# Kernel tuning notes

Measured on AMD Instinct MI355X. Metric: run time of the kernel, lower is better.

Reference implementation:

```python
import jax, jax.numpy as jnp
import numpy as np
import math

D_MODEL = 1024
NUM_HEADS = 16
HEAD_DIM = D_MODEL // NUM_HEADS


def _xavier(key, out_f, in_f):
    limit = math.sqrt(6.0 / (in_f + out_f))
    return jax.random.uniform(key, (out_f, in_f), jnp.float32, -limit, limit)


def ternarize(w):
    # abs-mean threshold -> {-1, 0, +1}
    abs_mean = jnp.mean(jnp.abs(w))
    return jnp.where(jnp.abs(w) > abs_mean, jnp.sign(w), jnp.zeros_like(w))


def setup_inputs() -> dict:
    key = jax.random.key(0)
    kq, kk, kv, kwq, kwk, kwv, kwo = jax.random.split(key, 7)
    B, S = 2, 2048
    return {
        "query": jax.random.normal(kq, (B, S, D_MODEL), jnp.float32),
        "key": jax.random.normal(kk, (B, S, D_MODEL), jnp.float32),
        "value": jax.random.normal(kv, (B, S, D_MODEL), jnp.float32),
        "w_q": _xavier(kwq, D_MODEL, D_MODEL),
        "w_k": _xavier(kwk, D_MODEL, D_MODEL),
        "w_v": _xavier(kwv, D_MODEL, D_MODEL),
        "w_o": _xavier(kwo, D_MODEL, D_MODEL),
    }


def reference(query, key, value, w_q, w_k, w_v, w_o):
    B, S, _ = query.shape
    # ternary projections (F.linear: x @ W.T)
    q = query @ ternarize(w_q).T
    k = key @ ternarize(w_k).T
    v = value @ ternarize(w_v).T
    # [B, H, S, Dh]
    q = q.reshape(B, S, NUM_HEADS, HEAD_DIM).transpose(0, 2, 1, 3)
    k = k.reshape(B, -1, NUM_HEADS, HEAD_DIM).transpose(0, 2, 1, 3)
    v = v.reshape(B, -1, NUM_HEADS, HEAD_DIM).transpose(0, 2, 1, 3)
    scores = jnp.einsum("bhqd,bhkd->bhqk", q, k) / math.sqrt(HEAD_DIM)
    probs = jax.nn.softmax(scores, axis=-1)
    out = jnp.einsum("bhqk,bhkd->bhqd", probs, v)
    out = out.transpose(0, 2, 1, 3).reshape(B, S, D_MODEL)
    return out @ ternarize(w_o).T
```

## Files before the change

kernel.cpp:

```cpp
#include <hip/hip_runtime.h>
#include <cstdint>
#include <cstddef>

typedef __bf16 bfloat;
typedef __bf16 bf16x8 __attribute__((ext_vector_type(8)));
typedef __bf16 bf16x4 __attribute__((ext_vector_type(4)));
typedef float  f32x4  __attribute__((ext_vector_type(4)));

static constexpr int D  = 1024;
static constexpr int S  = 2048;
static constexpr int B  = 2;
static constexpr int H  = 16;
static constexpr int DH = 64;
static constexpr int M  = B * S;
static constexpr int WMAT_N = 1024 * 1024;

#define MFMA_BF16(a, b, c) __builtin_amdgcn_mfma_f32_16x16x32_bf16((a), (b), (c), 0, 0, 0)

__device__ __forceinline__ void gl_lds16(const void* g, void* l) {
  __builtin_amdgcn_global_load_lds(
      (const __attribute__((address_space(1))) void*)g,
      (__attribute__((address_space(3))) void*)l, 16, 0, 0);
}

__global__ void prep_kernel(const float* __restrict__ w0, const float* __restrict__ w1,
                            const float* __restrict__ w2, const float* __restrict__ w3,
                            const float* __restrict__ qx, const float* __restrict__ kx,
                            const float* __restrict__ vx, bfloat* __restrict__ qhi,
                            bfloat* __restrict__ qlo, bfloat* __restrict__ khi,
                            bfloat* __restrict__ klo, bfloat* __restrict__ vhi,
                            double* __restrict__ sums) {
  const int y = blockIdx.y;
  if (y < 4) {
    const float* w = (y == 0) ? w0 : (y == 1) ? w1 : (y == 2) ? w2 : w3;
    const float4* w4 = (const float4*)w;
    double s = 0.0;
    for (int i = blockIdx.x * blockDim.x + threadIdx.x; i < (WMAT_N / 4);
         i += gridDim.x * blockDim.x) {
      float4 v = w4[i];
      s += (double)fabsf(v.x) + (double)fabsf(v.y) + (double)fabsf(v.z) + (double)fabsf(v.w);
    }
    for (int off = 1; off < 64; off <<= 1) s += __shfl_xor(s, off, 64);
    __shared__ double ps[4];
    if ((threadIdx.x & 63) == 0) ps[threadIdx.x >> 6] = s;
    __syncthreads();
    if (threadIdx.x == 0) atomicAdd(&sums[y], ps[0] + ps[1] + ps[2] + ps[3]);
  } else {
    const int z = y - 4;
    const float* x = (z == 0) ? qx : (z == 1) ? kx : vx;
    bfloat* hi = (z == 0) ? qhi : (z == 1) ? khi : vhi;
    bfloat* lo = (z == 0) ? qlo : (z == 1) ? klo : nullptr;
    const int n8 = M * D / 8;
    const float4* x4 = (const float4*)x;
    for (int i = blockIdx.x * blockDim.x + threadIdx.x; i < n8;
         i += gridDim.x * blockDim.x) {
      float4 a = x4[2 * i], b = x4[2 * i + 1];
      float f[8] = {a.x, a.y, a.z, a.w, b.x, b.y, b.z, b.w};
      bf16x8 h;
#pragma unroll
      for (int j = 0; j < 8; j++) h[j] = (bfloat)f[j];
      *(bf16x8*)&hi[(size_t)i * 8] = h;
      if (z < 2) {
        bf16x8 l;
#pragma unroll
        for (int j = 0; j < 8; j++) l[j] = (bfloat)(f[j] - (float)h[j]);
        *(bf16x8*)&lo[(size_t)i * 8] = l;
      }
    }
  }
}

__global__ void tern_kernel(const float* __restrict__ w0, const float* __restrict__ w1,
                            const float* __restrict__ w2, const float* __restrict__ w3,
                            bfloat* __restrict__ o0, bfloat* __restrict__ o1,
                            bfloat* __restrict__ o2, bfloat* __restrict__ o3,
                            const double* __restrict__ sums) {
  int z = blockIdx.y;
  const float* w = (z == 0) ? w0 : (z == 1) ? w1 : (z == 2) ? w2 : w3;
  bfloat* o = (z == 0) ? o0 : (z == 1) ? o1 : (z == 2) ? o2 : o3;
  double thr = sums[z] * (1.0 / (double)WMAT_N);
  const float4* w4 = (const float4*)w;
  for (int i = blockIdx.x * blockDim.x + threadIdx.x; i < (WMAT_N / 4);
       i += gridDim.x * blockDim.x) {
    float4 v = w4[i];
    bf16x4 r;
    r[0] = (bfloat)(((double)fabsf(v.x) > thr) ? (v.x > 0.f ? 1.f : -1.f) : 0.f);
    r[1] = (bfloat)(((double)fabsf(v.y) > thr) ? (v.y > 0.f ? 1.f : -1.f) : 0.f);
    r[2] = (bfloat)(((double)fabsf(v.z) > thr) ? (v.z > 0.f ? 1.f : -1.f) : 0.f);
    r[3] = (bfloat)(((double)fabsf(v.w) > thr) ? (v.w > 0.f ? 1.f : -1.f) : 0.f);
    *(bf16x4*)&o[(size_t)i * 4] = r;
  }
}

__global__ __launch_bounds__(256) void qkv_gemm(
    const bfloat* __restrict__ xqh, const bfloat* __restrict__ xql,
    const bfloat* __restrict__ xkh, const bfloat* __restrict__ xkl,
    const bfloat* __restrict__ xvh, const bfloat* __restrict__ wqt,
    const bfloat* __restrict__ wkt, const bfloat* __restrict__ wvt,
    bfloat* __restrict__ qmh, bfloat* __restrict__ qml,
    bfloat* __restrict__ kmh, bfloat* __restrict__ kml, bfloat* __restrict__ vtr) {
  constexpr int K = D;
  constexpr int N = D;
  __shared__ __align__(16) bfloat As0[128 * 64];
  __shared__ __align__(16) bfloat As1[128 * 64];
  __shared__ __align__(16) bfloat Ws[128 * 64];

  const int z = blockIdx.z;
  const bfloat *A0, *A1 = nullptr, *Wm;
  bfloat *Oh = nullptr, *Ol = nullptr;
  float scale = 1.f;
  bool split;
  if (z == 0) {
    A0 = xqh; A1 = xql; Wm = wqt; Oh = qmh; Ol = qml;
    scale = 0.18033688f;
    split = true;
  } else if (z == 1) {
    A0 = xkh; A1 = xkl; Wm = wkt; Oh = kmh; Ol = kml; split = true;
  } else {
    A0 = xvh; Wm = wvt; split = false;
  }

  const int t = threadIdx.x;
  const int w = t >> 6, lane = t & 63;
  const int quad = lane >> 4, l16 = lane & 15;
  const int wm = w >> 1, wn = w & 1;
  const int m0 = blockIdx.y * 128, n0 = blockIdx.x * 128;

  f32x4 acc[4][4] = {};

  const int srr = lane >> 3;
  const int spc = lane & 7;

  for (int kk = 0; kk < K; kk += 64) {
#pragma unroll
    for (int g = 0; g < 4; g++) {
      int row = w * 32 + g * 8 + srr;
      int cl = spc ^ (row & 7);
      int lo = (w * 32 + g * 8) * 64;
      gl_lds16(A0 + (size_t)(m0 + row) * K + kk + cl * 8, As0 + lo);
      if (split) gl_lds16(A1 + (size_t)(m0 + row) * K + kk + cl * 8, As1 + lo);
      gl_lds16(Wm + (size_t)(n0 + row) * K + kk + cl * 8, Ws + lo);
    }
    __syncthreads();

#pragma unroll
    for (int kidx = 0; kidx < 2; kidx++) {
      bf16x8 bfrag[4], afrag[4];
#pragma unroll
      for (int nt = 0; nt < 4; nt++) {
        int r = wn * 64 + nt * 16 + l16;
        bfrag[nt] = *(const bf16x8*)&Ws[r * 64 + (((kidx * 4 + quad) ^ (r & 7)) * 8)];
      }
#pragma unroll
      for (int mt = 0; mt < 4; mt++) {
        int r = wm * 64 + mt * 16 + l16;
        afrag[mt] = *(const bf16x8*)&As0[r * 64 + (((kidx * 4 + quad) ^ (r & 7)) * 8)];
      }
#pragma unroll
      for (int mt = 0; mt < 4; mt++)
#pragma unroll
        for (int nt = 0; nt < 4; nt++)
          acc[mt][nt] = MFMA_BF16(afrag[mt], bfrag[nt], acc[mt][nt]);
      if (split) {
#pragma unroll
        for (int mt = 0; mt < 4; mt++) {
          int r = wm * 64 + mt * 16 + l16;
          afrag[mt] = *(const bf16x8*)&As1[r * 64 + (((kidx * 4 + quad) ^ (r & 7)) * 8)];
        }
#pragma unroll
        for (int mt = 0; mt < 4; mt++)
#pragma unroll
          for (int nt = 0; nt < 4; nt++)
            acc[mt][nt] = MFMA_BF16(afrag[mt], bfrag[nt], acc[mt][nt]);
      }
    }
    __syncthreads();
  }

#pragma unroll
  for (int mt = 0; mt < 4; mt++) {
#pragma unroll
    for (int nt = 0; nt < 4; nt++) {
      const int row = m0 + wm * 64 + mt * 16 + quad * 4;
      const int col = n0 + wn * 64 + nt * 16 + l16;
      if (split) {
#pragma unroll
        for (int rg = 0; rg < 4; rg++) {
          float vv = acc[mt][nt][rg] * scale;
          size_t idx = (size_t)(row + rg) * N + col;
          bfloat hh = (bfloat)vv;
          Oh[idx] = hh;
          Ol[idx] = (bfloat)(vv - (float)hh);
        }
      } else {
        int bb = row >> 11, s = row & (S - 1);
        int kk6 = s & 63;
        int pos = (kk6 & 3) | (((kk6 >> 4) & 1) << 2) | (((kk6 >> 2) & 3) << 3) |
                  ((kk6 >> 5) << 5);
        int sp = (s & ~63) | pos;
        bf16x4 pk;
#pragma unroll
        for (int rg = 0; rg < 4; rg++) pk[rg] = (bfloat)acc[mt][nt][rg];
        *(bf16x4*)&vtr[(size_t)bb * D * S + (size_t)col * S + sp] = pk;
      }
    }
  }
}

__global__ __launch_bounds__(256, 4) void gemm_wo(const bfloat* __restrict__ A,
                                                  const bfloat* __restrict__ Wm,
                                                  float* __restrict__ Cf) {
  constexpr int K = D;
  constexpr int N = D;
  __shared__ __align__(16) bfloat As[64 * 64];
  __shared__ __align__(16) bfloat Ws[64 * 64];

  const int t = threadIdx.x;
  const int w = t >> 6, lane = t & 63;
  const int quad = lane >> 4, l16 = lane & 15;
  const int wm = w >> 1, wn = w & 1;
  const int m0 = blockIdx.y * 64, n0 = blockIdx.x * 64;

  f32x4 acc[2][2] = {};

  const int srr = lane >> 3;
  const int spc = lane & 7;

  for (int kk = 0; kk < K; kk += 64) {
#pragma unroll
    for (int g = 0; g < 2; g++) {
      int row = w * 16 + g * 8 + srr;
      int cl = spc ^ (row & 7);
      int lo = (w * 16 + g * 8) * 64;
      gl_lds16(A + (size_t)(m0 + row) * K + kk + cl * 8, As + lo);
      gl_lds16(Wm + (size_t)(n0 + row) * K + kk + cl * 8, Ws + lo);
    }
    __syncthreads();

#pragma unroll
    for (int kidx = 0; kidx < 2; kidx++) {
      bf16x8 af[2], bfr[2];
#pragma unroll
      for (int i = 0; i < 2; i++) {
        int ar = wm * 32 + i * 16 + l16;
        af[i] = *(const bf16x8*)&As[ar * 64 + (((kidx * 4 + quad) ^ (ar & 7)) * 8)];
        int br = wn * 32 + i * 16 + l16;
        bfr[i] = *(const bf16x8*)&Ws[br * 64 + (((kidx * 4 + quad) ^ (br & 7)) * 8)];
      }
#pragma unroll
      for (int mt = 0; mt < 2; mt++)
#pragma unroll
        for (int nt = 0; nt < 2; nt++)
          acc[mt][nt] = MFMA_BF16(af[mt], bfr[nt], acc[mt][nt]);
    }
    __syncthreads();
  }

#pragma unroll
  for (int mt = 0; mt < 2; mt++) {
#pragma unroll
    for (int nt = 0; nt < 2; nt++) {
      const int row = m0 + wm * 32 + mt * 16 + quad * 4;
      const int col = n0 + wn * 32 + nt * 16 + l16;
#pragma unroll
      for (int rg = 0; rg < 4; rg++) Cf[(size_t)(row + rg) * N + col] = acc[mt][nt][rg];
    }
  }
}

__global__ __launch_bounds__(256) void flash_kernel(
    const bfloat* __restrict__ qh, const bfloat* __restrict__ ql,
    const bfloat* __restrict__ kh, const bfloat* __restrict__ kl,
    const bfloat* __restrict__ vt, bfloat* __restrict__ outp) {
  __shared__ __align__(16) bfloat Kh[64 * 64];
  __shared__ __align__(16) bfloat Kl[64 * 64];
  __shared__ __align__(16) bfloat Vt[64 * 64];

  const int t = threadIdx.x;
  const int w = t >> 6, lane = t & 63;
  const int quad = lane >> 4, l16 = lane & 15;
  const int b = blockIdx.z, h = blockIdx.y;
  const int q0 = blockIdx.x * 64;
  const size_t base = (size_t)b * S * D + (size_t)h * DH;
  const size_t vbase = (size_t)b * D * S + (size_t)h * DH * S;

  const int ssr = lane >> 3;
  const int spc = lane & 7;

  bf16x8 ones;
#pragma unroll
  for (int j = 0; j < 8; j++) ones[j] = (bfloat)1.f;

#pragma unroll
  for (int g = 0; g < 2; g++) {
    int r = w * 16 + g * 8 + ssr;
    int c = spc ^ (r & 7);
    int lo = (w * 16 + g * 8) * 64;
    gl_lds16(qh + base + (size_t)(q0 + r) * D + c * 8, Kh + lo);
    gl_lds16(ql + base + (size_t)(q0 + r) * D + c * 8, Kl + lo);
  }
  __syncthreads();
  bf16x8 qhf[2], qlf[2];
  {
    int row = w * 16 + l16;
#pragma unroll
    for (int s2 = 0; s2 < 2; s2++) {
      qhf[s2] = *(const bf16x8*)&Kh[row * 64 + (((s2 * 4 + quad) ^ (l16 & 7)) * 8)];
      qlf[s2] = *(const bf16x8*)&Kl[row * 64 + (((s2 * 4 + quad) ^ (l16 & 7)) * 8)];
    }
  }
  __syncthreads();

  f32x4 Oa[4] = {};
  f32x4 La = {};
  float m_i = -3.0e38f;

  for (int k0 = 0; k0 < S; k0 += 64) {
#pragma unroll
    for (int g = 0; g < 2; g++) {
      int r = w * 16 + g * 8 + ssr;
      int c = spc ^ (r & 7);
      int lo = (w * 16 + g * 8) * 64;
      gl_lds16(kh + base + (size_t)(k0 + r) * D + c * 8, Kh + lo);
      gl_lds16(kl + base + (size_t)(k0 + r) * D + c * 8, Kl + lo);
      gl_lds16(vt + vbase + (size_t)r * S + k0 + c * 8, Vt + lo);
    }
    __syncthreads();

    f32x4 sf[4];
#pragma unroll
    for (int mt = 0; mt < 4; mt++) {
      f32x4 a = {};
      int krow = mt * 16 + l16;
#pragma unroll
      for (int s2 = 0; s2 < 2; s2++) {
        bf16x8 bh = *(const bf16x8*)&Kh[krow * 64 + (((s2 * 4 + quad) ^ (l16 & 7)) * 8)];
        bf16x8 bl = *(const bf16x8*)&Kl[krow * 64 + (((s2 * 4 + quad) ^ (l16 & 7)) * 8)];
        a = MFMA_BF16(bh, qhf[s2], a);
        a = MFMA_BF16(bl, qhf[s2], a);
        a = MFMA_BF16(bh, qlf[s2], a);
      }
      sf[mt] = a;
    }

    float mm = sf[0][0];
#pragma unroll
    for (int mt = 0; mt < 4; mt++)
#pragma unroll
      for (int rg = 0; rg < 4; rg++) mm = fmaxf(mm, sf[mt][rg]);
    mm = fmaxf(mm, __shfl_xor(mm, 16, 64));
    mm = fmaxf(mm, __shfl_xor(mm, 32, 64));
    if (__ballot(mm > m_i)) {
      float mnew = fmaxf(m_i, mm);
      float alpha = exp2f(m_i - mnew);
      m_i = mnew;
#pragma unroll
      for (int mt = 0; mt < 4; mt++) Oa[mt] *= alpha;
      La *= alpha;
    }
#pragma unroll
    for (int mt = 0; mt < 4; mt++)
#pragma unroll
      for (int rg = 0; rg < 4; rg++) sf[mt][rg] = exp2f(sf[mt][rg] - m_i);

#pragma unroll
    for (int kp = 0; kp < 2; kp++) {
      bf16x8 pb8;
#pragma unroll
      for (int rg = 0; rg < 4; rg++) {
        pb8[rg]     = (bfloat)sf[2 * kp][rg];
        pb8[4 + rg] = (bfloat)sf[2 * kp + 1][rg];
      }
      La = MFMA_BF16(ones, pb8, La);
#pragma unroll
      for (int mt = 0; mt < 4; mt++) {
        int vrow = mt * 16 + l16;
        bf16x8 va = *(const bf16x8*)&Vt[vrow * 64 + (((kp * 4 + quad) ^ (vrow & 7)) * 8)];
        Oa[mt] = MFMA_BF16(va, pb8, Oa[mt]);
      }
    }
    __syncthreads();
  }

  float inv = 1.0f / La[0];
  const int qrow = q0 + w * 16 + l16;
#pragma unroll
  for (int mt = 0; mt < 4; mt++) {
    bf16x4 ov;
#pragma unroll
    for (int rg = 0; rg < 4; rg++) ov[rg] = (bfloat)(Oa[mt][rg] * inv);
    *(bf16x4*)&outp[base + (size_t)qrow * D + mt * 16 + quad * 4] = ov;
  }
}

extern "C" void kernel_launch(void* const* d_in, const int* in_sizes, int n_in,
                              void* d_out, int out_size, void* d_ws, size_t ws_size,
                              hipStream_t stream) {
  const float* q_in = (const float*)d_in[0];
  const float* k_in = (const float*)d_in[1];
  const float* v_in = (const float*)d_in[2];
  const float* wq = (const float*)d_in[3];
  const float* wk = (const float*)d_in[4];
  const float* wv = (const float*)d_in[5];
  const float* wo = (const float*)d_in[6];
  float* outp = (float*)d_out;
  char* ws = (char*)d_ws;

  constexpr size_t WBYTES = (size_t)WMAT_N * 2;
  constexpr size_t XBYTES = (size_t)M * D * 2;
  size_t off = 0;
  double* sums = (double*)(ws + off); off += 256;
  bfloat* wqt = (bfloat*)(ws + off); off += WBYTES;
  bfloat* wkt = (bfloat*)(ws + off); off += WBYTES;
  bfloat* wvt = (bfloat*)(ws + off); off += WBYTES;
  bfloat* wot = (bfloat*)(ws + off); off += WBYTES;
  bfloat* xqh = (bfloat*)(ws + off); off += XBYTES;
  bfloat* xql = (bfloat*)(ws + off); off += XBYTES;
  bfloat* xkh = (bfloat*)(ws + off); off += XBYTES;
  bfloat* xkl = (bfloat*)(ws + off); off += XBYTES;
  bfloat* xvh = (bfloat*)(ws + off); off += XBYTES;
  bfloat* qmh = (bfloat*)(ws + off); off += XBYTES;
  bfloat* qml = (bfloat*)(ws + off); off += XBYTES;
  bfloat* kmh = (bfloat*)(ws + off); off += XBYTES;
  bfloat* kml = (bfloat*)(ws + off); off += XBYTES;
  bfloat* vtr = (bfloat*)(ws + off); off += XBYTES;
  bfloat* attn = xqh;

  hipMemsetAsync(sums, 0, 4 * sizeof(double), stream);
  prep_kernel<<<dim3(256, 7), 256, 0, stream>>>(
      wq, wk, wv, wo, q_in, k_in, v_in, xqh, xql, xkh, xkl, xvh, sums);
  tern_kernel<<<dim3(128, 4), 256, 0, stream>>>(wq, wk, wv, wo, wqt, wkt, wvt, wot, sums);
  qkv_gemm<<<dim3(D / 128, M / 128, 3), 256, 0, stream>>>(
      xqh, xql, xkh, xkl, xvh, wqt, wkt, wvt, qmh, qml, kmh, kml, vtr);
  flash_kernel<<<dim3(S / 64, H, B), 256, 0, stream>>>(qmh, qml, kmh, kml, vtr, attn);
  gemm_wo<<<dim3(D / 64, M / 64), 256, 0, stream>>>(attn, wot, outp);
}
```

Baseline: 295.6 us.

## Double-buffer K tiles and overlap V load with QK in flash attention

Restructures the flash attention loop into a single shared buffer with double-buffered K hi/lo tiles and a separate V tile. The next K tile and the current V tile are prefetched before the QK MFMAs, with manual vmcnt waits and raw barriers in place of __syncthreads. It also raises wave priority around MFMA sections and skips the rescale unless the running max grows by more than 8 (lazy rescaling). The extra LDS use may lower occupancy, and the hand-placed waitcnt and barrier ordering must be correct for the results to stay valid.

After: 300.8 us. About the same (+1.8%).

```diff
diff --git a/kernel.cpp b/kernel.cpp
--- a/kernel.cpp
+++ b/kernel.cpp
@@ -272,12 +272,10 @@
     const bfloat* __restrict__ qh, const bfloat* __restrict__ ql,
     const bfloat* __restrict__ kh, const bfloat* __restrict__ kl,
     const bfloat* __restrict__ vt, bfloat* __restrict__ outp) {
-  __shared__ __align__(16) bfloat Kh[64 * 64];
-  __shared__ __align__(16) bfloat Kl[64 * 64];
-  __shared__ __align__(16) bfloat Vt[64 * 64];
-
-  const int t = threadIdx.x;
-  const int w = t >> 6, lane = t & 63;
+  __shared__ __align__(16) bfloat SM[20480];
+
+  const int tid = threadIdx.x;
+  const int w = tid >> 6, lane = tid & 63;
   const int quad = lane >> 4, l16 = lane & 15;
   const int b = blockIdx.z, h = blockIdx.y;
   const int q0 = blockIdx.x * 64;
@@ -286,71 +284,94 @@
 
   const int ssr = lane >> 3;
   const int spc = lane & 7;
+  const int c8 = (spc ^ ssr) * 8;
+  const int stK = w * 16 * 64;
+
+  const bfloat* pQh = qh + base + (size_t)(q0 + w * 16 + ssr) * D + c8;
+  const bfloat* pQl = ql + base + (size_t)(q0 + w * 16 + ssr) * D + c8;
+  const bfloat* pKh = kh + base + (size_t)(w * 16 + ssr) * D + c8;
+  const bfloat* pKl = kl + base + (size_t)(w * 16 + ssr) * D + c8;
+  const bfloat* pV = vt + vbase + (size_t)(w * 16 + ssr) * S + c8;
 
   bf16x8 ones;
 #pragma unroll
   for (int j = 0; j < 8; j++) ones[j] = (bfloat)1.f;
 
-#pragma unroll
-  for (int g = 0; g < 2; g++) {
-    int r = w * 16 + g * 8 + ssr;
-    int c = spc ^ (r & 7);
-    int lo = (w * 16 + g * 8) * 64;
-    gl_lds16(qh + base + (size_t)(q0 + r) * D + c * 8, Kh + lo);
-    gl_lds16(ql + base + (size_t)(q0 + r) * D + c * 8, Kl + lo);
-  }
-  __syncthreads();
-  bf16x8 qhf[2], qlf[2];
-  {
-    int row = w * 16 + l16;
-#pragma unroll
-    for (int s2 = 0; s2 < 2; s2++) {
-      qhf[s2] = *(const bf16x8*)&Kh[row * 64 + (((s2 * 4 + quad) ^ (l16 & 7)) * 8)];
-      qlf[s2] = *(const bf16x8*)&Kl[row * 64 + (((s2 * 4 + quad) ^ (l16 & 7)) * 8)];
-    }
-  }
-  __syncthreads();
+  gl_lds16(pQh, SM + 8192 + stK);
+  gl_lds16(pQh + 8 * D, SM + 8192 + stK + 512);
+  gl_lds16(pQl, SM + 12288 + stK);
+  gl_lds16(pQl + 8 * D, SM + 12288 + stK + 512);
+  asm volatile("s_waitcnt vmcnt(0)" ::: "memory");
+  __builtin_amdgcn_s_barrier();
+  asm volatile("" ::: "memory");
+
+  const int fo0 = l16 * 64 + ((quad ^ (l16 & 7)) * 8);
+  const int fo4 = fo0 ^ 32;
+  const int fq = w * 1024;
+
+  gl_lds16(pKh, SM + 0 + stK);
+  gl_lds16(pKh + 8 * D, SM + 0 + stK + 512);
+  gl_lds16(pKl, SM + 4096 + stK);
+  gl_lds16(pKl + 8 * D, SM + 4096 + stK + 512);
+  pKh += 64 * D;
+  pKl += 64 * D;
+
+  bf16x8 qhf0 = *(const bf16x8*)&SM[8192 + fq + fo0];
+  bf16x8 qhf1 = *(const bf16x8*)&SM[8192 + fq + fo4];
+  bf16x8 qlf0 = *(const bf16x8*)&SM[12288 + fq + fo0];
+  bf16x8 qlf1 = *(const bf16x8*)&SM[12288 + fq + fo4];
+  asm volatile("s_waitcnt lgkmcnt(0) vmcnt(0)" ::: "memory");
 
   f32x4 Oa[4] = {};
   f32x4 La = {};
   float m_i = -3.0e38f;
-
-  for (int k0 = 0; k0 < S; k0 += 64) {
-#pragma unroll
-    for (int g = 0; g < 2; g++) {
-      int r = w * 16 + g * 8 + ssr;
-      int c = spc ^ (r & 7);
-      int lo = (w * 16 + g * 8) * 64;
-      gl_lds16(kh + base + (size_t)(k0 + r) * D + c * 8, Kh + lo);
-      gl_lds16(kl + base + (size_t)(k0 + r) * D + c * 8, Kl + lo);
-      gl_lds16(vt + vbase + (size_t)r * S + k0 + c * 8, Vt + lo);
-    }
-    __syncthreads();
+  constexpr int NT = S / 64;
+
+  for (int t = 0; t < NT; ++t) {
+    __builtin_amdgcn_s_barrier();
+    asm volatile("" ::: "memory");
+    const int cur = (t & 1) * 8192;
+    const int nxt = 8192 - cur;
+
+    gl_lds16(pV, SM + 16384 + stK);
+    gl_lds16(pV + 8 * S, SM + 16384 + stK + 512);
+    pV += 64;
+    if (t < NT - 1) {
+      gl_lds16(pKh, SM + nxt + stK);
+      gl_lds16(pKh + 8 * D, SM + nxt + stK + 512);
+      gl_lds16(pKl, SM + nxt + 4096 + stK);
+      gl_lds16(pKl + 8 * D, SM + nxt + 4096 + stK + 512);
+      pKh += 64 * D;
+      pKl += 64 * D;
+    }
 
     f32x4 sf[4];
+    __builtin_amdgcn_s_setprio(1);
 #pragma unroll
     for (int mt = 0; mt < 4; mt++) {
       f32x4 a = {};
-      int krow = mt * 16 + l16;
-#pragma unroll
-      for (int s2 = 0; s2 < 2; s2++) {
-        bf16x8 bh = *(const bf16x8*)&Kh[krow * 64 + (((s2 * 4 + quad) ^ (l16 & 7)) * 8)];
-        bf16x8 bl = *(const bf16x8*)&Kl[krow * 64 + (((s2 * 4 + quad) ^ (l16 & 7)) * 8)];
-        a = MFMA_BF16(bh, qhf[s2], a);
-        a = MFMA_BF16(bl, qhf[s2], a);
-        a = MFMA_BF16(bh, qlf[s2], a);
-      }
+      bf16x8 bh0 = *(const bf16x8*)&SM[cur + fo0 + mt * 1024];
+      bf16x8 bl0 = *(const bf16x8*)&SM[cur + 4096 + fo0 + mt * 1024];
+      bf16x8 bh1 = *(const bf16x8*)&SM[cur + fo4 + mt * 1024];
+      bf16x8 bl1 = *(const bf16x8*)&SM[cur + 4096 + fo4 + mt * 1024];
+      a = MFMA_BF16(bh0, qhf0, a);
+      a = MFMA_BF16(bl0, qhf0, a);
+      a = MFMA_BF16(bh0, qlf0, a);
+      a = MFMA_BF16(bh1, qhf1, a);
+      a = MFMA_BF16(bl1, qhf1, a);
+      a = MFMA_BF16(bh1, qlf1, a);
       sf[mt] = a;
     }
-
-    float mm = sf[0][0];
-#pragma unroll
-    for (int mt = 0; mt < 4; mt++)
-#pragma unroll
-      for (int rg = 0; rg < 4; rg++) mm = fmaxf(mm, sf[mt][rg]);
+    __builtin_amdgcn_s_setprio(0);
+
+    float t0 = fmaxf(fmaxf(sf[0][0], sf[0][1]), fmaxf(sf[0][2], sf[0][3]));
+    float t1 = fmaxf(fmaxf(sf[1][0], sf[1][1]), fmaxf(sf[1][2], sf[1][3]));
+    float t2 = fmaxf(fmaxf(sf[2][0], sf[2][1]), fmaxf(sf[2][2], sf[2][3]));
+    float t3 = fmaxf(fmaxf(sf[3][0], sf[3][1]), fmaxf(sf[3][2], sf[3][3]));
+    float mm = fmaxf(fmaxf(t0, t1), fmaxf(t2, t3));
     mm = fmaxf(mm, __shfl_xor(mm, 16, 64));
     mm = fmaxf(mm, __shfl_xor(mm, 32, 64));
-    if (__ballot(mm > m_i)) {
+    if (__ballot(mm > m_i + 8.0f)) {
       float mnew = fmaxf(m_i, mm);
       float alpha = exp2f(m_i - mnew);
       m_i = mnew;
@@ -363,23 +384,32 @@
 #pragma unroll
       for (int rg = 0; rg < 4; rg++) sf[mt][rg] = exp2f(sf[mt][rg] - m_i);
 
+    if (t < NT - 1)
+      asm volatile("s_waitcnt vmcnt(4)" ::: "memory");
+    else
+      asm volatile("s_waitcnt vmcnt(0)" ::: "memory");
+    __builtin_amdgcn_s_barrier();
+    asm volatile("" ::: "memory");
+
+    __builtin_amdgcn_s_setprio(1);
 #pragma unroll
     for (int kp = 0; kp < 2; kp++) {
       bf16x8 pb8;
 #pragma unroll
       for (int rg = 0; rg < 4; rg++) {
-        pb8[rg]     = (bfloat)sf[2 * kp][rg];
+        pb8[rg] = (bfloat)sf[2 * kp][rg];
         pb8[4 + rg] = (bfloat)sf[2 * kp + 1][rg];
       }
       La = MFMA_BF16(ones, pb8, La);
+      const int fv = kp ? fo4 : fo0;
 #pragma unroll
       for (int mt = 0; mt < 4; mt++) {
-        int vrow = mt * 16 + l16;
-        bf16x8 va = *(const bf16x8*)&Vt[vrow * 64 + (((kp * 4 + quad) ^ (vrow & 7)) * 8)];
+        bf16x8 va = *(const bf16x8*)&SM[16384 + fv + mt * 1024];
         Oa[mt] = MFMA_BF16(va, pb8, Oa[mt]);
       }
     }
-    __syncthreads();
+    __builtin_amdgcn_s_setprio(0);
+    asm volatile("s_waitcnt vmcnt(0)" ::: "memory");
   }
 
   float inv = 1.0f / La[0];
```
